# Optimization experiments

Hardware: AMD Instinct MI355X
Metric: run time of the kernel (lower is better)

The kernel has to match this reference:

```python
import jax, jax.numpy as jnp
import numpy as np

T = 64
NBITS_PSUM = 8
NBITS_ACC = 8
K = 2
EPS = 1e-5

def _binarize_ste(x):
    # sign binarization with straight-through estimator (torch code overwrites .data)
    s = jnp.where(x >= 0, 1.0, -1.0).astype(x.dtype)
    return x + jax.lax.stop_gradient(s - x)

def _binary_conv_psum(x, w):
    # x: [N,C,H,W], w: [O,C,3,3]. Binarized 3x3 conv (stride 1, pad 1) computed as
    # chunks of T products along the unrolled reduction dim, each partial sum
    # quantized to NBITS_PSUM bits with step K, final accumulator clipped to NBITS_ACC.
    N, C, H, W = x.shape
    O = w.shape[0]
    xb = _binarize_ste(x)
    wb = _binarize_ste(w)
    patches = jax.lax.conv_general_dilated_patches(
        xb, (3, 3), (1, 1), ((1, 1), (1, 1)),
        dimension_numbers=('NCHW', 'OIHW', 'NCHW'))  # [N, C*9, H, W], channel-major
    R = C * 9
    nch = R // T  # 2304 / 64 = 36 chunks
    p = patches.reshape(N, nch, T, H, W).transpose(1, 0, 2, 3, 4)  # [nch,N,T,H,W]
    wf = wb.reshape(O, nch, T).transpose(1, 0, 2)                   # [nch,O,T]
    qmax = 2 ** (NBITS_PSUM - 1) - 1
    step = float(K)

    def body(carry, xs):
        acc, reg = carry
        pc, wc = xs
        psum = jnp.einsum('nthw,ot->nohw', pc, wc)  # partial sum over T binary products
        q = jnp.clip(jnp.round(psum / step), -qmax - 1, qmax) * step
        q_ste = psum + jax.lax.stop_gradient(q - psum)  # STE through quantizer
        reg = reg + jnp.mean((q - psum) ** 2)  # quantization-error regularizer
        return (acc + q_ste, reg), None

    acc0 = jnp.zeros((N, O, H, W), x.dtype)
    (acc, reg), _ = jax.lax.scan(body, (acc0, jnp.zeros((), x.dtype)), (p, wf))
    amax = (2 ** (NBITS_ACC - 1) - 1) * step  # accumulator clipping
    return jnp.clip(acc, -amax, amax), reg

def _bn(x, gamma, beta):
    # BatchNorm2d in training mode (batch statistics)
    m = jnp.mean(x, (0, 2, 3), keepdims=True)
    v = jnp.var(x, (0, 2, 3), keepdims=True)
    return (x - m) * jax.lax.rsqrt(v + EPS) * gamma[None, :, None, None] + beta[None, :, None, None]

def setup_inputs():
    key = jax.random.key(0)
    k1, k2, k3 = jax.random.split(key, 3)
    N, C, H, W = 32, 256, 32, 32
    return {
        'x0': jax.random.normal(k1, (N, C, H, W), jnp.float32),
        'reg0': jnp.zeros((), jnp.float32),
        'w1': jax.random.normal(k2, (C, C, 3, 3), jnp.float32),
        'gamma1': jnp.ones((C,), jnp.float32),
        'beta1': jnp.zeros((C,), jnp.float32),
        'w2': jax.random.normal(k3, (C, C, 3, 3), jnp.float32),
        'gamma2': jnp.ones((C,), jnp.float32),
        'beta2': jnp.zeros((C,), jnp.float32),
    }

def reference(x0, reg0, w1, gamma1, beta1, w2, gamma2, beta2):
    residual = x0
    out, r1 = _binary_conv_psum(x0, w1)
    reg = reg0 + r1
    out = _bn(out, gamma1, beta1)
    out = jnp.clip(out, -1.0, 1.0)  # Hardtanh
    out, r2 = _binary_conv_psum(out, w2)
    reg = reg + r2
    out = out + residual  # downsample is None
    reg = reg + r2        # faithful to original: conv2's r is added again after residual
    out = _bn(out, gamma2, beta2)
    out = jnp.clip(out, -1.0, 1.0)  # Hardtanh (do_bntan=True)
    return out, reg
```

## Files before the change

kernel.cpp:

```cpp
#include <hip/hip_runtime.h>

typedef unsigned long long u64;
typedef __attribute__((ext_vector_type(4)))  int i32x4;
typedef __attribute__((ext_vector_type(16))) int i32x16;

#define NPIX   32768
#define OCH    256
#define NCH    36

#define AROWS  196
#define ALDS   (AROWS * 256)
#define BLDS   8192
#define GLDS   (ALDS + 3 * BLDS)

__device__ __forceinline__ void gload16(const void* g, void* l) {
  __builtin_amdgcn_global_load_lds(
      (const __attribute__((address_space(1))) unsigned*)g,
      (__attribute__((address_space(3))) unsigned*)l, 16, 0, 0);
}

__global__ __launch_bounds__(256) void bb_pre(const float* __restrict__ wa,
                                              const float* __restrict__ wb,
                                              const float* __restrict__ x,
                                              u64* __restrict__ Wbits,
                                              signed char* __restrict__ B,
                                              float* __restrict__ st,
                                              u64* __restrict__ masks,
                                              u64* __restrict__ Sb,
                                              signed char* __restrict__ A) {
  __shared__ float xt[256][33];
  int blk = blockIdx.x, t = threadIdx.x;
  if (blk == 0) {
    for (int i = t; i < 1024; i += 256) st[i] = 0.f;
    for (int id = t; id < 9 * NCH; id += 256) {
      int cls = id / NCH, ck = id % NCH;
      int ch = cls / 3, cw = cls % 3;
      u64 m = 0;
      for (int b = 0; b < 64; ++b) {
        int r = ck * 64 + b, tap = r % 9, kh = tap / 3, kw = tap % 3;
        bool oob = (ch == 0 && kh == 0) || (ch == 2 && kh == 2) ||
                   (cw == 0 && kw == 0) || (cw == 2 && kw == 2);
        if (!oob) m |= (u64)1 << b;
      }
      masks[id] = m;
    }
  } else if (blk <= 4608) {
    int word = (((blk - 1) << 8) + t) >> 6;
    int ln = t & 63;
    const float* src = (word < OCH * NCH) ? wa : wb;
    int r = word % (OCH * NCH);
    u64 bits = __ballot(src[(size_t)r * 64 + ln] >= 0.f);
    int l = word / (OCH * NCH);
    int o = r / NCH, ck = r % NCH;
    if (ln == 0) Wbits[(size_t)l * OCH * NCH + (size_t)ck * OCH + o] = bits;
  } else if (blk <= 9216) {
    int tid = ((blk - 4609) << 8) + t;
    int l = tid >= 589824;
    int r = l ? tid - 589824 : tid;
    const float* src = l ? wb : wa;
    float v = src[r];
    int tp = r % 9, oc9 = r / 9;
    int c = oc9 & 255, o = oc9 >> 8;
    B[(((size_t)(l * 9 + tp) * 256 + o) << 8) + c] = (v >= 0.f) ? 1 : -1;
  } else {
    int bx = blk - 9217;
    int n = bx >> 5, h = bx & 31;
    int w = t & 31, cg = t >> 5;
    for (int k = 0; k < 32; ++k) {
      int c = k * 8 + cg;
      xt[c][w] = x[((size_t)((n * 256 + c) * 32 + h) << 5) + w];
    }
    __syncthreads();
    int ln = t & 63, wv = t >> 6;
    int c2 = wv * 64 + ln;
    for (int w2 = 0; w2 < 32; ++w2) {
      bool s = xt[c2][w2] >= 0.f;
      u64 bits = __ballot(s);
      int px = (n * 32 + h) * 32 + w2;
      A[(size_t)px * 256 + c2] = s ? 1 : -1;
      if (ln == 0) Sb[(size_t)px * 4 + wv] = bits;
    }
  }
}

__global__ __launch_bounds__(256, 2) void bb_conv(const signed char* __restrict__ A,
                                                  const signed char* __restrict__ B,
                                                  const u64* __restrict__ Sb,
                                                  const u64* __restrict__ Wb,
                                                  const u64* __restrict__ masks,
                                                  short* __restrict__ dst) {
  extern __shared__ signed char sm[];
  int bx = blockIdx.x, t = threadIdx.x;
  if (bx < 512) {
    int wv = t >> 6, ln = t & 63;
    int lw = ln & 31, hk = ln >> 5;
    int px0 = (bx >> 1) << 7;
    int oc0 = (bx & 1) << 7;

    const signed char* Abase = A + (size_t)(px0 - 33) * 256;
    #pragma unroll
    for (int i = 0; i < 13; ++i) {
      int c = i * 4 + wv;
      if (c < 49) {
        int u = c * 64 + ln;
        int row = u >> 4, p = u & 15;
        gload16(Abase + (size_t)row * 256 + (((p ^ (row & 7)) << 4)),
                &sm[c * 1024]);
      }
    }

    #define STAGE_B(bufi, ks) do {                                            \
      int tp_ = (ks) >> 2, cb_ = (ks) & 3;                                    \
      const signed char* Bb_ = B + ((size_t)tp_ << 16) + (size_t)oc0 * 256    \
                                 + (cb_ << 6);                                \
      _Pragma("unroll")                                                       \
      for (int i_ = 0; i_ < 2; ++i_) {                                        \
        int c_ = wv * 2 + i_;                                                 \
        int u_ = c_ * 64 + ln;                                                \
        int row_ = u_ >> 2, p_ = u_ & 3;                                      \
        gload16(Bb_ + (size_t)row_ * 256 + (((p_ ^ ((row_ >> 1) & 3)) << 4)), \
                &sm[ALDS + (bufi) * BLDS + c_ * 1024]);                       \
      }                                                                       \
    } while (0)

    STAGE_B(0, 0);
    STAGE_B(1, 1);
    asm volatile("s_waitcnt vmcnt(2)" ::: "memory");
    __builtin_amdgcn_s_barrier();

    int wm = wv >> 1, wn = wv & 1;
    int arow0 = 33 + (wm << 6) + lw;
    int brow0 = (wn << 6) + lw;
    i32x16 acc00 = {0,0,0,0,0,0,0,0,0,0,0,0,0,0,0,0};
    i32x16 acc01 = acc00, acc10 = acc00, acc11 = acc00;

    for (int ks = 0; ks < 36; ++ks) {
      if (ks + 2 < 36) STAGE_B((ks + 2) % 3, ks + 2);
      int tp = ks >> 2, cb = ks & 3;
      int dpx = (tp / 3 - 1) * 32 + (tp % 3 - 1);
      int r0 = arow0 + dpx, r1 = r0 + 32;
      int q0 = brow0, q1 = brow0 + 32;
      const signed char* Bl = sm + ALDS + (ks % 3) * BLDS;
      __builtin_amdgcn_s_setprio(1);
      #pragma unroll
      for (int k32 = 0; k32 < 2; ++k32) {
        int sa = cb * 4 + k32 * 2 + hk;
        int sb = k32 * 2 + hk;
        i32x4 a0 = *(const i32x4*)(sm + r0 * 256 + ((sa ^ (r0 & 7)) << 4));
        i32x4 a1 = *(const i32x4*)(sm + r1 * 256 + ((sa ^ (r1 & 7)) << 4));
        i32x4 b0 = *(const i32x4*)(Bl + q0 * 64 + ((sb ^ ((q0 >> 1) & 3)) << 4));
        i32x4 b1 = *(const i32x4*)(Bl + q1 * 64 + ((sb ^ ((q1 >> 1) & 3)) << 4));
        acc00 = __builtin_amdgcn_mfma_i32_32x32x32_i8(a0, b0, acc00, 0, 0, 0);
        acc01 = __builtin_amdgcn_mfma_i32_32x32x32_i8(a0, b1, acc01, 0, 0, 0);
        acc10 = __builtin_amdgcn_mfma_i32_32x32x32_i8(a1, b0, acc10, 0, 0, 0);
        acc11 = __builtin_amdgcn_mfma_i32_32x32x32_i8(a1, b1, acc11, 0, 0, 0);
      }
      __builtin_amdgcn_s_setprio(0);
      if (ks < 34) asm volatile("s_waitcnt vmcnt(2)" ::: "memory");
      else         asm volatile("s_waitcnt vmcnt(0)" ::: "memory");
      __builtin_amdgcn_s_barrier();
    }
    #undef STAGE_B

    int px0w = px0 + (wm << 6), oc0w = oc0 + (wn << 6);
    int rbase = hk << 2;
    int h0 = (px0w >> 5) & 31, h1 = ((px0w + 32) >> 5) & 31;
    bool i0 = (h0 >= 1) && (h0 <= 30);
    bool i1 = (h1 >= 1) && (h1 <= 30);
    #pragma unroll
    for (int r = 0; r < 16; ++r) {
      int m = (r & 3) + ((r >> 2) << 3) + rbase;
      bool wok = (m >= 1) && (m <= 30);
      size_t row0 = ((size_t)(px0w + m)) << 8;
      size_t row1 = ((size_t)(px0w + 32 + m)) << 8;
      int v;
      if (i0 && wok) {
        v = acc00[r]; v = v < -254 ? -254 : (v > 254 ? 254 : v);
        dst[row0 + oc0w + lw] = (short)v;
        v = acc01[r]; v = v < -254 ? -254 : (v > 254 ? 254 : v);
        dst[row0 + oc0w + 32 + lw] = (short)v;
      }
      if (i1 && wok) {
        v = acc10[r]; v = v < -254 ? -254 : (v > 254 ? 254 : v);
        dst[row1 + oc0w + lw] = (short)v;
        v = acc11[r]; v = v < -254 ? -254 : (v > 254 ? 254 : v);
        dst[row1 + oc0w + 32 + lw] = (short)v;
      }
    }
    return;
  }

  u64* spread = (u64*)sm;
  u64* pw     = spread + 256;
  u64* mm     = pw + 16 * NCH;
  int* pm     = (int*)(mm + 16 * NCH);
  int* pxl    = pm + 16 * NCH;
  {
    u64 v = 0;
    for (int k = 0; k < 8; ++k) if (t & (1 << k)) v |= (u64)1 << (9 * k);
    spread[t] = v;
  }
  __syncthreads();
  int bb = bx - 512;
  for (int id = t; id < 16 * NCH; id += 256) {
    int p = id / NCH, ck = id % NCH;
    int gp = bb * 16 + p;
    int n = gp / 124, r = gp % 124;
    int h, w;
    if (r < 32)      { h = 0;      w = r;      }
    else if (r < 64) { h = 31;     w = r - 32; }
    else if (r < 94) { h = r - 63; w = 0;      }
    else             { h = r - 93; w = 31;     }
    int cls = (h == 0 ? 0 : (h == 31 ? 2 : 1)) * 3 + (w == 0 ? 0 : (w == 31 ? 2 : 1));
    if (ck == 0) pxl[p] = ((n * 32 + h) << 5) + w;
    int base9 = ck % 9;
    u64 acc = 0;
    for (int tap = 0; tap < 9; ++tap) {
      int b0 = tap - base9; if (b0 < 0) b0 += 9;
      int nh = h + tap / 3 - 1, nw = w + tap % 3 - 1;
      if ((unsigned)nh <= 31u && (unsigned)nw <= 31u) {
        int run = (b0 == 0) ? 8 : 7;
        int c0 = (ck * 64 + b0) / 9;
        const u64* rp = Sb + ((size_t)((n * 32 + nh) * 32 + nw) << 2);
        int wi = c0 >> 6, sh = c0 & 63;
        u64 v = rp[wi] >> sh;
        if (sh + run > 64) v |= rp[wi + 1] << (64 - sh);
        v &= (run == 8) ? 0xFFull : 0x7Full;
        acc |= spread[(int)v] << b0;
      }
    }
    pw[p * NCH + ck] = acc;
    u64 m = masks[cls * NCH + ck];
    mm[p * NCH + ck] = m;
    pm[p * NCH + ck] = __popcll(m);
  }
  __syncthreads();
  int oc = t;
  int acc[16];
  #pragma unroll
  for (int p = 0; p < 16; ++p) acc[p] = 0;
  for (int i = 0; i < NCH; ++i) {
    u64 wr = Wb[(size_t)i * OCH + oc];
    #pragma unroll
    for (int p = 0; p < 16; ++p) {
      int d = __popcll((pw[p * NCH + i] ^ wr) & mm[p * NCH + i]);
      int ps = pm[p * NCH + i] - 2 * d;
      acc[p] += ps + (ps & 1) * ((ps & 2) - 1);
    }
  }
  #pragma unroll
  for (int p = 0; p < 16; ++p) {
    int v = acc[p];
    v = v < -254 ? -254 : (v > 254 ? 254 : v);
    dst[(size_t)pxl[p] * OCH + oc] = (short)v;
  }
}

__global__ void bb_stats1(const short* v16, float* st) {
  int t = threadIdx.x;
  const short* base = v16 + (size_t)blockIdx.x * 128 * OCH;
  int s = 0; float q = 0.f;
  for (int r = 0; r < 128; ++r) {
    int v = base[r * OCH + t];
    s += v; q += (float)(v * v);
  }
  atomicAdd(&st[t], (float)s);
  atomicAdd(&st[256 + t], q);
}

__global__ void bb_xbits2(const short* v16, const float* st,
                          const float* g, const float* b, u64* Sb,
                          signed char* A) {
  int wave = (blockIdx.x * blockDim.x + threadIdx.x) >> 6;
  int ln = threadIdx.x & 63;
  int wrd = wave & 3, px0 = (wave >> 2) * 32;
  int oc = wrd * 64 + ln;
  float mu = st[oc] * (1.f / 32768.f);
  float va = st[256 + oc] * (1.f / 32768.f) - mu * mu;
  float rs = rsqrtf(va + 1e-5f);
  float gg = g[oc], bb = b[oc];
  for (int j = 0; j < 32; ++j) {
    float bn = ((float)v16[(size_t)(px0 + j) * OCH + oc] - mu) * rs * gg + bb;
    bool s = bn >= 0.f;
    u64 bits = __ballot(s);
    A[(size_t)(px0 + j) * 256 + oc] = s ? 1 : -1;
    if (ln == 0) Sb[(size_t)(px0 + j) * 4 + wrd] = bits;
  }
}

__global__ __launch_bounds__(256) void bb_stats2t(const short* __restrict__ pre16,
                                                  const float* __restrict__ x0,
                                                  float* st) {
  __shared__ float xt[32][257];
  int blk = blockIdx.x;
  int n = blk >> 5, h = blk & 31;
  int t = threadIdx.x;
  int w = t & 31, og = t >> 5;
  for (int k = 0; k < 32; ++k) {
    int oc = og * 32 + k;
    xt[w][oc] = x0[((size_t)(n * 256 + oc) * 32 + h) * 32 + w];
  }
  __syncthreads();
  int oc = t;
  size_t pb = (size_t)blk * 32 * OCH + oc;
  float s = 0.f, q = 0.f;
  for (int w2 = 0; w2 < 32; ++w2) {
    float v = (float)pre16[pb + (size_t)w2 * OCH] + xt[w2][oc];
    s += v; q += v * v;
  }
  atomicAdd(&st[512 + oc], s);
  atomicAdd(&st[768 + oc], q);
}

__global__ __launch_bounds__(256) void bb_fint(const short* __restrict__ pre16,
                                               const float* __restrict__ x0,
                                               const float* st, const float* g,
                                               const float* b, const float* r0,
                                               float* __restrict__ out) {
  __shared__ float xt[32][257];
  int blk = blockIdx.x;
  int n = blk >> 5, h = blk & 31;
  int t = threadIdx.x;
  int w = t & 31, og = t >> 5;
  for (int k = 0; k < 32; ++k) {
    int oc = og * 32 + k;
    xt[w][oc] = x0[((size_t)(n * 256 + oc) * 32 + h) * 32 + w];
  }
  __syncthreads();
  int oc = t;
  float mu = st[512 + oc] * (1.f / 32768.f);
  float va = st[768 + oc] * (1.f / 32768.f) - mu * mu;
  float rs = rsqrtf(va + 1e-5f);
  float gg = g[oc], bb = b[oc];
  size_t pb = (size_t)blk * 32 * OCH + oc;
  for (int w2 = 0; w2 < 32; ++w2) {
    float v = (float)pre16[pb + (size_t)w2 * OCH] + xt[w2][oc];
    v = (v - mu) * rs * gg + bb;
    xt[w2][oc] = fminf(fmaxf(v, -1.f), 1.f);
  }
  __syncthreads();
  for (int k = 0; k < 32; ++k) {
    int oc2 = og * 32 + k;
    out[((size_t)(n * 256 + oc2) * 32 + h) * 32 + w] = xt[w][oc2];
  }
  if (blk == 0 && t == 0) out[8388608] = r0[0] + 8.625f;
}

extern "C" void kernel_launch(void* const* d_in, const int* in_sizes, int n_in,
                              void* d_out, int out_size, void* d_ws, size_t ws_size,
                              hipStream_t stream) {
  const float* x0   = (const float*)d_in[0];
  const float* reg0 = (const float*)d_in[1];
  const float* w1   = (const float*)d_in[2];
  const float* g1   = (const float*)d_in[3];
  const float* b1   = (const float*)d_in[4];
  const float* w2   = (const float*)d_in[5];
  const float* g2   = (const float*)d_in[6];
  const float* b2   = (const float*)d_in[7];

  char* ws = (char*)d_ws;
  u64*   Wbits = (u64*)(ws);
  u64*   masks = (u64*)(ws + 147456);
  float* st    = (float*)(ws + 151552);
  u64*   Sb    = (u64*)(ws + 155648);
  signed char* Bi8 = (signed char*)(ws + 1204224);
  signed char* Ai8 = (signed char*)(ws + 2383872) + 32768;
  short* v16   = (short*)(ws + 10838016);

  bb_pre    <<<10241, 256, 0, stream>>>(w1, w2, x0, Wbits, Bi8, st, masks,
                                        Sb, Ai8);
  bb_conv   <<<760, 256, GLDS, stream>>>(Ai8, Bi8, Sb, Wbits, masks, v16);
  bb_stats1 <<<256, 256, 0, stream>>>(v16, st);
  bb_xbits2 <<<1024, 256, 0, stream>>>(v16, st, g1, b1, Sb, Ai8);
  bb_conv   <<<760, 256, GLDS, stream>>>(Ai8, Bi8 + 589824, Sb,
                                         Wbits + OCH * NCH, masks, v16);
  bb_stats2t<<<1024, 256, 0, stream>>>(v16, x0, st);
  bb_fint   <<<1024, 256, 0, stream>>>(v16, x0, st, g2, b2, reg0, (float*)d_out);
}
```

Before: 283.4 us.

## Load binarized weights directly from global into registers, dropping LDS B staging

```diff
diff --git a/kernel.cpp b/kernel.cpp
--- a/kernel.cpp
+++ b/kernel.cpp
@@ -10,8 +10,6 @@
 
 #define AROWS  196
 #define ALDS   (AROWS * 256)
-#define BLDS   8192
-#define GLDS   (ALDS + 3 * BLDS)
 
 __device__ __forceinline__ void gload16(const void* g, void* l) {
   __builtin_amdgcn_global_load_lds(
@@ -61,7 +59,9 @@
     float v = src[r];
     int tp = r % 9, oc9 = r / 9;
     int c = oc9 & 255, o = oc9 >> 8;
-    B[(((size_t)(l * 9 + tp) * 256 + o) << 8) + c] = (v >= 0.f) ? 1 : -1;
+    int cb = c >> 6, s = (c >> 4) & 3, j = c & 15;
+    B[(((size_t)((l * 9 + tp) * 16 + cb * 4 + s)) << 12) + (o << 4) + j] =
+        (v >= 0.f) ? 1 : -1;
   } else {
     int bx = blk - 9217;
     int n = bx >> 5, h = bx & 31;
@@ -108,59 +108,35 @@
                 &sm[c * 1024]);
       }
     }
-
-    #define STAGE_B(bufi, ks) do {                                            \
-      int tp_ = (ks) >> 2, cb_ = (ks) & 3;                                    \
-      const signed char* Bb_ = B + ((size_t)tp_ << 16) + (size_t)oc0 * 256    \
-                                 + (cb_ << 6);                                \
-      _Pragma("unroll")                                                       \
-      for (int i_ = 0; i_ < 2; ++i_) {                                        \
-        int c_ = wv * 2 + i_;                                                 \
-        int u_ = c_ * 64 + ln;                                                \
-        int row_ = u_ >> 2, p_ = u_ & 3;                                      \
-        gload16(Bb_ + (size_t)row_ * 256 + (((p_ ^ ((row_ >> 1) & 3)) << 4)), \
-                &sm[ALDS + (bufi) * BLDS + c_ * 1024]);                       \
-      }                                                                       \
-    } while (0)
-
-    STAGE_B(0, 0);
-    STAGE_B(1, 1);
-    asm volatile("s_waitcnt vmcnt(2)" ::: "memory");
+    asm volatile("s_waitcnt vmcnt(0)" ::: "memory");
     __builtin_amdgcn_s_barrier();
 
     int wm = wv >> 1, wn = wv & 1;
     int arow0 = 33 + (wm << 6) + lw;
-    int brow0 = (wn << 6) + lw;
+    const signed char* Bp = B + (((size_t)(oc0 + (wn << 6) + lw)) << 4)
+                              + (hk << 12);
     i32x16 acc00 = {0,0,0,0,0,0,0,0,0,0,0,0,0,0,0,0};
     i32x16 acc01 = acc00, acc10 = acc00, acc11 = acc00;
 
+    #pragma unroll 4
     for (int ks = 0; ks < 36; ++ks) {
-      if (ks + 2 < 36) STAGE_B((ks + 2) % 3, ks + 2);
       int tp = ks >> 2, cb = ks & 3;
       int dpx = (tp / 3 - 1) * 32 + (tp % 3 - 1);
       int r0 = arow0 + dpx, r1 = r0 + 32;
-      int q0 = brow0, q1 = brow0 + 32;
-      const signed char* Bl = sm + ALDS + (ks % 3) * BLDS;
-      __builtin_amdgcn_s_setprio(1);
       #pragma unroll
       for (int k32 = 0; k32 < 2; ++k32) {
         int sa = cb * 4 + k32 * 2 + hk;
-        int sb = k32 * 2 + hk;
         i32x4 a0 = *(const i32x4*)(sm + r0 * 256 + ((sa ^ (r0 & 7)) << 4));
         i32x4 a1 = *(const i32x4*)(sm + r1 * 256 + ((sa ^ (r1 & 7)) << 4));
-        i32x4 b0 = *(const i32x4*)(Bl + q0 * 64 + ((sb ^ ((q0 >> 1) & 3)) << 4));
-        i32x4 b1 = *(const i32x4*)(Bl + q1 * 64 + ((sb ^ ((q1 >> 1) & 3)) << 4));
+        i32x4 b0 = *(const i32x4*)(Bp + (k32 << 13));
+        i32x4 b1 = *(const i32x4*)(Bp + (k32 << 13) + 512);
         acc00 = __builtin_amdgcn_mfma_i32_32x32x32_i8(a0, b0, acc00, 0, 0, 0);
         acc01 = __builtin_amdgcn_mfma_i32_32x32x32_i8(a0, b1, acc01, 0, 0, 0);
         acc10 = __builtin_amdgcn_mfma_i32_32x32x32_i8(a1, b0, acc10, 0, 0, 0);
         acc11 = __builtin_amdgcn_mfma_i32_32x32x32_i8(a1, b1, acc11, 0, 0, 0);
       }
-      __builtin_amdgcn_s_setprio(0);
-      if (ks < 34) asm volatile("s_waitcnt vmcnt(2)" ::: "memory");
-      else         asm volatile("s_waitcnt vmcnt(0)" ::: "memory");
-      __builtin_amdgcn_s_barrier();
-    }
-    #undef STAGE_B
+      Bp += 16384;
+    }
 
     int px0w = px0 + (wm << 6), oc0w = oc0 + (wn << 6);
     int rbase = hk << 2;
@@ -369,10 +345,10 @@
 
   bb_pre    <<<10241, 256, 0, stream>>>(w1, w2, x0, Wbits, Bi8, st, masks,
                                         Sb, Ai8);
-  bb_conv   <<<760, 256, GLDS, stream>>>(Ai8, Bi8, Sb, Wbits, masks, v16);
+  bb_conv   <<<760, 256, ALDS, stream>>>(Ai8, Bi8, Sb, Wbits, masks, v16);
   bb_stats1 <<<256, 256, 0, stream>>>(v16, st);
   bb_xbits2 <<<1024, 256, 0, stream>>>(v16, st, g1, b1, Sb, Ai8);
-  bb_conv   <<<760, 256, GLDS, stream>>>(Ai8, Bi8 + 589824, Sb,
+  bb_conv   <<<760, 256, ALDS, stream>>>(Ai8, Bi8 + 589824, Sb,
                                          Wbits + OCH * NCH, masks, v16);
   bb_stats2t<<<1024, 256, 0, stream>>>(v16, x0, st);
   bb_fint   <<<1024, 256, 0, stream>>>(v16, x0, st, g2, b2, reg0, (float*)d_out);
```

Measured after the change: 257.5 us. 9.2% less time.
